# Kernel tuning notes

Hardware: AMD Instinct MI355X
Metric: run time of the kernel (lower is better)

Reference implementation:

```python
import jax, jax.numpy as jnp
import numpy as np

N_NODES = 50000
N_EDGES = 800000
N_GRAPHS = 128
HEADS = 4
HDIM = 32
N_CLASSES = 10
LEAKY_ALPHA = 0.2


def setup_inputs() -> dict:
    key = jax.random.key(0)
    ks = jax.random.split(key, 12)
    src = jax.random.randint(ks[0], (N_EDGES,), 0, N_NODES, dtype=jnp.int32)
    # guarantee every node has in-degree >= 1 so 3/deg is finite
    dst_tail = jax.random.randint(ks[1], (N_EDGES - N_NODES,), 0, N_NODES, dtype=jnp.int32)
    dst = jnp.concatenate([jnp.arange(N_NODES, dtype=jnp.int32), dst_tail])
    graph_ids = jnp.sort(jax.random.randint(ks[2], (N_NODES,), 0, N_GRAPHS, dtype=jnp.int32))
    s = 0.1
    return {
        "src": src,
        "dst": dst,
        "graph_ids": graph_ids,
        "W1": jax.random.normal(ks[3], (4, HEADS * HDIM), jnp.float32) * s,
        "al1": jax.random.normal(ks[4], (HEADS, HDIM), jnp.float32) * s,
        "ar1": jax.random.normal(ks[5], (HEADS, HDIM), jnp.float32) * s,
        "W2": jax.random.normal(ks[6], (HEADS * HDIM, HEADS * HDIM), jnp.float32) * s,
        "al2": jax.random.normal(ks[7], (HEADS, HDIM), jnp.float32) * s,
        "ar2": jax.random.normal(ks[8], (HEADS, HDIM), jnp.float32) * s,
        "Wc": jax.random.normal(ks[9], (HEADS * HDIM, N_CLASSES), jnp.float32) * s,
        "bc": jax.random.normal(ks[10], (N_CLASSES,), jnp.float32) * s,
    }


def _gat_layer(x, src, dst, W, al, ar):
    # x: [N, Fin]; W: [Fin, H*D]; al, ar: [H, D]
    n = x.shape[0]
    ft = (x @ W).reshape(n, HEADS, HDIM)                       # [N, H, D]
    a1 = jnp.einsum("nhd,hd->nh", ft, al)                      # [N, H]
    a2 = jnp.einsum("nhd,hd->nh", ft, ar)                      # [N, H]
    e = jax.nn.leaky_relu(a1[src] + a2[dst], LEAKY_ALPHA)      # [E, H]
    # segment softmax over incoming edges of each dst node
    m = jax.ops.segment_max(e, dst, num_segments=n)            # [N, H]
    m = jax.lax.stop_gradient(m)
    ex = jnp.exp(e - m[dst])                                   # [E, H]
    denom = jax.ops.segment_sum(ex, dst, num_segments=n)       # [N, H]
    alpha = ex / denom[dst]                                    # [E, H]
    # gather-multiply-scatter aggregation
    out = jax.ops.segment_sum(ft[src] * alpha[:, :, None], dst, num_segments=n)  # [N, H, D]
    return jax.nn.relu(out.reshape(n, HEADS * HDIM))


def reference(src, dst, graph_ids, W1, al1, ar1, W2, al2, ar2, Wc, bc):
    n = N_NODES
    ones_e = jnp.ones(src.shape[0], jnp.float32)
    deg = jax.ops.segment_sum(ones_e, dst, num_segments=n)     # in-degrees [N]
    h = jnp.stack(
        [deg, (deg - 3.0 > 0).astype(jnp.float32), 3.0 / deg, (deg - 4.0 > 0).astype(jnp.float32)],
        axis=1,
    )                                                          # [N, 4]
    h = _gat_layer(h, src, dst, W1, al1, ar1)                  # [N, H*D]
    h = _gat_layer(h, src, dst, W2, al2, ar2)                  # [N, H*D]
    # mean_nodes: per-graph mean pooling
    gsum = jax.ops.segment_sum(h, graph_ids, num_segments=N_GRAPHS)
    cnt = jax.ops.segment_sum(jnp.ones(n, jnp.float32), graph_ids, num_segments=N_GRAPHS)
    gmean = gsum / jnp.maximum(cnt, 1.0)[:, None]              # [G, H*D]
    return jax.nn.sigmoid(gmean @ Wc + bc)                     # [G, n_classes]
```

## Files before the change

### kernel.cpp

```cpp
#include <hip/hip_runtime.h>
#include <hip/hip_fp16.h>
#include <math.h>

#define HEADS 4
#define HDIM 32
#define FDIM 128
#define NGRAPH 128
#define NCLASS 10

#define NBW 128
#define NBP 512
#define SLICE 4096

typedef _Float16 h4_t __attribute__((ext_vector_type(4)));
typedef float f4_t __attribute__((ext_vector_type(4)));
typedef float f2_t __attribute__((ext_vector_type(2)));

__device__ __forceinline__ float lrelu(float x) { return fmaxf(x, 0.2f * x); }

__global__ void k_zb(int* __restrict__ bcnt) {
    int i = threadIdx.x;
    bcnt[i] = 0; bcnt[i + 256] = 0;
}

__global__ void k_bhist(const int* __restrict__ dst, int E, int* __restrict__ bcnt) {
    __shared__ int lcnt[NBP];
    int tid = threadIdx.x;
    for (int i = tid; i < NBP; i += 256) lcnt[i] = 0;
    __syncthreads();
    int beg = blockIdx.x * SLICE, end = min(E, beg + SLICE);
    for (int i = beg + tid; i < end; i += 256)
        atomicAdd(&lcnt[dst[i] >> 7], 1);
    __syncthreads();
    for (int i = tid; i < NBP; i += 256)
        if (lcnt[i]) atomicAdd(&bcnt[i], lcnt[i]);
}

__global__ void k_bscan2(const int* __restrict__ bcnt, int* __restrict__ bbase,
                         int* __restrict__ bcur) {
    __shared__ int ws[4];
    int tid = threadIdx.x, lane = tid & 63, w = tid >> 6;
    int c0 = bcnt[2 * tid], c1 = bcnt[2 * tid + 1];
    int t = c0 + c1;
    int incl = t;
    #pragma unroll
    for (int off = 1; off < 64; off <<= 1) {
        int y = __shfl_up(incl, off);
        if (lane >= off) incl += y;
    }
    if (lane == 63) ws[w] = incl;
    __syncthreads();
    int wpre = 0;
    #pragma unroll
    for (int j = 0; j < 4; ++j) if (j < w) wpre += ws[j];
    int ex = wpre + (incl - t);
    bbase[2 * tid] = ex;          bcur[2 * tid] = ex;
    bbase[2 * tid + 1] = ex + c0; bcur[2 * tid + 1] = ex + c0;
}

__global__ __launch_bounds__(256) void k_part(const int* __restrict__ src,
        const int* __restrict__ dst, int E, int* __restrict__ bcur,
        int2* __restrict__ part) {
    __shared__ int lcnt[NBP];
    __shared__ int loff[NBP];
    __shared__ int lpos[NBP];
    __shared__ int2 staged[SLICE];
    __shared__ int tgt[SLICE];
    __shared__ int ws[4];
    int tid = threadIdx.x, lane = tid & 63, w = tid >> 6;
    int beg = blockIdx.x * SLICE, end = min(E, beg + SLICE);
    int m = end - beg;
    for (int i = tid; i < NBP; i += 256) lcnt[i] = 0;
    __syncthreads();
    for (int i = beg + tid; i < end; i += 256)
        atomicAdd(&lcnt[dst[i] >> 7], 1);
    __syncthreads();
    int c0 = lcnt[2 * tid], c1 = lcnt[2 * tid + 1];
    int t = c0 + c1;
    int incl = t;
    #pragma unroll
    for (int off = 1; off < 64; off <<= 1) {
        int y = __shfl_up(incl, off);
        if (lane >= off) incl += y;
    }
    if (lane == 63) ws[w] = incl;
    __syncthreads();
    int wpre = 0;
    #pragma unroll
    for (int j = 0; j < 4; ++j) if (j < w) wpre += ws[j];
    int ex = wpre + (incl - t);
    loff[2 * tid] = ex; loff[2 * tid + 1] = ex + c0;
    if (c0) lpos[2 * tid] = atomicAdd(&bcur[2 * tid], c0);
    if (c1) lpos[2 * tid + 1] = atomicAdd(&bcur[2 * tid + 1], c1);
    lcnt[2 * tid] = 0; lcnt[2 * tid + 1] = 0;
    __syncthreads();
    for (int i = beg + tid; i < end; i += 256) {
        int s = src[i], d = dst[i];
        int b = d >> 7;
        int idx = atomicAdd(&lcnt[b], 1);
        int slot = loff[b] + idx;
        staged[slot] = make_int2(s, d);
        tgt[slot] = lpos[b] + idx;
    }
    __syncthreads();
    for (int i = tid; i < m; i += 256)
        part[tgt[i]] = staged[i];
}

__global__ __launch_bounds__(256) void k_build(const int2* __restrict__ part,
        const int* __restrict__ bbase, const int* __restrict__ bcnt,
        int* __restrict__ deg, int* __restrict__ offs, int* __restrict__ csr,
        int n, int E) {
    __shared__ int ldeg[NBW];
    __shared__ int loffs[NBW];
    __shared__ int wtot[2];
    int b = blockIdx.x, tid = threadIdx.x;
    int lane = tid & 63, w = tid >> 6;
    if (tid < NBW) ldeg[tid] = 0;
    __syncthreads();
    int beg = bbase[b], end = beg + bcnt[b];
    for (int i = beg + tid; i < end; i += 256)
        atomicAdd(&ldeg[part[i].y & (NBW - 1)], 1);
    __syncthreads();
    int x = (tid < NBW) ? ldeg[tid] : 0;
    int incl = x;
    #pragma unroll
    for (int off = 1; off < 64; off <<= 1) {
        int y = __shfl_up(incl, off);
        if (lane >= off) incl += y;
    }
    if (tid < NBW && lane == 63) wtot[w] = incl;
    __syncthreads();
    if (tid < NBW) {
        int pre = incl - x;
        if (w == 1) pre += wtot[0];
        loffs[tid] = beg + pre;
        int v = b * NBW + tid;
        if (v < n) { deg[v] = x; offs[v] = beg + pre; }
    }
    if (b == 0 && tid == 0) offs[n] = E;
    __syncthreads();
    if (tid < NBW) ldeg[tid] = 0;
    __syncthreads();
    for (int i = beg + tid; i < end; i += 256) {
        int2 e = part[i];
        int lv = e.y & (NBW - 1);
        int p = atomicAdd(&ldeg[lv], 1);
        csr[loffs[lv] + p] = e.x;
    }
}

__global__ void k_atts1(const int* __restrict__ deg, const float* __restrict__ W1,
                        const float* __restrict__ al, const float* __restrict__ ar,
                        float* __restrict__ h4t, float* __restrict__ a1,
                        float* __restrict__ a2, int n) {
    __shared__ float wla[16], wlr[16];
    int tid = threadIdx.x;
    if (tid < 32) {
        int k = (tid & 15) >> 2, h = tid & 3;
        const float* av = (tid < 16) ? al : ar;
        float s = 0.f;
        #pragma unroll
        for (int d = 0; d < 32; ++d) s += W1[k * FDIM + h * HDIM + d] * av[h * HDIM + d];
        if (tid < 16) wla[k * 4 + h] = s; else wlr[k * 4 + h] = s;
    }
    __syncthreads();
    int v = blockIdx.x * blockDim.x + tid;
    if (v >= n) return;
    float d = (float)deg[v];
    float4 hv = make_float4(d, (d - 3.0f > 0.0f) ? 1.0f : 0.0f, 3.0f / d,
                            (d - 4.0f > 0.0f) ? 1.0f : 0.0f);
    *(float4*)(h4t + v * 4) = hv;
    float4 o1, o2;
    #pragma unroll
    for (int h = 0; h < 4; ++h) {
        float s1 = hv.x * wla[0 + h] + hv.y * wla[4 + h] + hv.z * wla[8 + h] + hv.w * wla[12 + h];
        float s2 = hv.x * wlr[0 + h] + hv.y * wlr[4 + h] + hv.z * wlr[8 + h] + hv.w * wlr[12 + h];
        if (h == 0) { o1.x = s1; o2.x = s2; } else if (h == 1) { o1.y = s1; o2.y = s2; }
        else if (h == 2) { o1.z = s1; o2.z = s2; } else { o1.w = s1; o2.w = s2; }
    }
    *(float4*)(a1 + v * 4) = o1;
    *(float4*)(a2 + v * 4) = o2;
}

__global__ void k_agg1(const int* __restrict__ offs, const int* __restrict__ csr,
                       const float* __restrict__ h4t, const float* __restrict__ a1,
                       const float* __restrict__ a2, float* __restrict__ S, int n) {
    int tid = threadIdx.x, lane = tid & 63, w = tid >> 6;
    int g = lane >> 4, e = lane & 15;
    int v = (blockIdx.x * 4 + w) * 4 + g;
    bool vok = v < n;
    int beg = 0, end = 0;
    if (vok) { beg = offs[v]; end = offs[v + 1]; }
    int deg = end - beg;
    float4 a2v = vok ? *(const float4*)(a2 + v * 4) : make_float4(0, 0, 0, 0);
    float P[4][4]; float D[4];
    #pragma unroll
    for (int h = 0; h < 4; ++h) { D[h] = 0.f;
        #pragma unroll
        for (int d = 0; d < 4; ++d) P[h][d] = 0.f; }
    for (int base = 0; base < deg; base += 16) {
        if (base + e < deg) {
            int u = csr[beg + base + e];
            float4 a1u = *(const float4*)(a1 + u * 4);
            float4 f4  = *(const float4*)(h4t + u * 4);
            float wgt[4];
            wgt[0] = __expf(lrelu(a1u.x + a2v.x));
            wgt[1] = __expf(lrelu(a1u.y + a2v.y));
            wgt[2] = __expf(lrelu(a1u.z + a2v.z));
            wgt[3] = __expf(lrelu(a1u.w + a2v.w));
            #pragma unroll
            for (int h = 0; h < 4; ++h) {
                D[h] += wgt[h];
                P[h][0] = fmaf(wgt[h], f4.x, P[h][0]);
                P[h][1] = fmaf(wgt[h], f4.y, P[h][1]);
                P[h][2] = fmaf(wgt[h], f4.z, P[h][2]);
                P[h][3] = fmaf(wgt[h], f4.w, P[h][3]);
            }
        }
    }
    #pragma unroll
    for (int off = 1; off < 16; off <<= 1) {
        #pragma unroll
        for (int h = 0; h < 4; ++h) {
            D[h] += __shfl_xor(D[h], off);
            #pragma unroll
            for (int d = 0; d < 4; ++d) P[h][d] += __shfl_xor(P[h][d], off);
        }
    }
    if (vok && e == 0) {
        #pragma unroll
        for (int h = 0; h < 4; ++h) {
            float r = 1.0f / D[h];
            *(float4*)(S + v * 16 + h * 4) =
                make_float4(P[h][0] * r, P[h][1] * r, P[h][2] * r, P[h][3] * r);
        }
    }
}

__global__ void k_wfrag(const float* __restrict__ W2, __half* __restrict__ Wfrag,
                        float* __restrict__ gsum, int* __restrict__ gcnt) {
    int gid = blockIdx.x * 256 + threadIdx.x;
    ((float4*)gsum)[gid] = make_float4(0.f, 0.f, 0.f, 0.f);
    if (gid < NGRAPH) gcnt[gid] = 0;
    int fid = gid >> 6, l = gid & 63;
    int ks = fid >> 3, t = fid & 7;
    int k0 = ks * 16 + 4 * (l >> 4);
    int n0 = t * 16 + (l & 15);
    __half2 lo = __floats2half2_rn(W2[(k0 + 0) * FDIM + n0], W2[(k0 + 1) * FDIM + n0]);
    __half2 hi = __floats2half2_rn(W2[(k0 + 2) * FDIM + n0], W2[(k0 + 3) * FDIM + n0]);
    size_t base = ((size_t)fid * 64 + l) * 4;
    *(__half2*)(Wfrag + base)     = lo;
    *(__half2*)(Wfrag + base + 2) = hi;
}

__global__ __launch_bounds__(256) void k_layer2(const float* __restrict__ S,
        const float* __restrict__ W1, const __half* __restrict__ Wfrag,
        const float* __restrict__ al, const float* __restrict__ ar,
        unsigned char* __restrict__ ft8, float* __restrict__ a1,
        float* __restrict__ a2, int n) {
    __shared__ __half Blds[64 * 64 * 4];
    __shared__ __half Alds[4][16 * 132];
    int tid = threadIdx.x, l = tid & 63, w = tid >> 6;
    int c = l & 15, g = l >> 4;

    #pragma unroll
    for (int i = 0; i < 8; ++i)
        ((float4*)Blds)[i * 256 + tid] = ((const float4*)Wfrag)[i * 256 + tid];

    int v0 = (blockIdx.x * 4 + w) * 16;
    float2 w1c[4];
    #pragma unroll
    for (int d = 0; d < 4; ++d) w1c[d] = *(const float2*)(W1 + d * FDIM + 2 * l);
    for (int jj = 0; jj < 16; ++jj) {
        int v = min(v0 + jj, n - 1);
        float4 s = *(const float4*)(S + v * 16 + g * 4);
        float t0 = s.x * w1c[0].x + s.y * w1c[1].x + s.z * w1c[2].x + s.w * w1c[3].x;
        float t1 = s.x * w1c[0].y + s.y * w1c[1].y + s.z * w1c[2].y + s.w * w1c[3].y;
        *(__half2*)(&Alds[w][jj * 132 + 2 * l]) = __floats2half2_rn(fmaxf(t0, 0.f), fmaxf(t1, 0.f));
    }
    __syncthreads();

    f4_t acc[8];
    #pragma unroll
    for (int t = 0; t < 8; ++t) acc[t] = (f4_t){0.f, 0.f, 0.f, 0.f};
    #pragma unroll
    for (int ks = 0; ks < 8; ++ks) {
        h4_t af = *(const h4_t*)(&Alds[w][c * 132 + ks * 16 + 4 * g]);
        #pragma unroll
        for (int t = 0; t < 8; ++t) {
            h4_t bf = *(const h4_t*)(&Blds[((ks * 8 + t) * 64 + l) * 4]);
            acc[t] = __builtin_amdgcn_mfma_f32_16x16x16f16(af, bf, acc[t], 0, 0, 0);
        }
    }

    #pragma unroll
    for (int t = 0; t < 8; ++t) {
        #pragma unroll
        for (int r = 0; r < 4; ++r) {
            int v = v0 + 4 * g + r;
            if (v < n) {
                int pk = __builtin_amdgcn_cvt_pk_fp8_f32(acc[t][r], acc[t][r], 0, false);
                ft8[(size_t)v * FDIM + t * 16 + c] = (unsigned char)(pk & 0xff);
            }
        }
    }
    float al0[4], al1v[4], ar0[4], ar1v[4];
    #pragma unroll
    for (int h = 0; h < 4; ++h) {
        al0[h] = al[h * 32 + c]; al1v[h] = al[h * 32 + 16 + c];
        ar0[h] = ar[h * 32 + c]; ar1v[h] = ar[h * 32 + 16 + c];
    }
    #pragma unroll
    for (int r = 0; r < 4; ++r) {
        int v = v0 + 4 * g + r;
        #pragma unroll
        for (int h = 0; h < 4; ++h) {
            float p1 = acc[2 * h][r] * al0[h] + acc[2 * h + 1][r] * al1v[h];
            float p2 = acc[2 * h][r] * ar0[h] + acc[2 * h + 1][r] * ar1v[h];
            #pragma unroll
            for (int off = 1; off < 16; off <<= 1) {
                p1 += __shfl_xor(p1, off);
                p2 += __shfl_xor(p2, off);
            }
            if (c == h && v < n) {
                a1[v * 4 + h] = p1;
                a2[v * 4 + h] = p2;
            }
        }
    }
}

__global__ void k_agg2(const int* __restrict__ offs, const int* __restrict__ csr,
                       const unsigned char* __restrict__ ft8, const float* __restrict__ a1,
                       const float* __restrict__ a2, __half* __restrict__ out, int n) {
    __shared__ float wlds[4][64 * 4];
    int tid = threadIdx.x, lane = tid & 63, w = tid >> 6;
    int v = blockIdx.x * 4 + w;
    if (v >= n) return;
    int beg = offs[v], end = offs[v + 1];
    int deg = end - beg;
    float4 a2v = *(const float4*)(a2 + v * 4);
    int h = lane >> 4;
    int f = 2 * lane;
    float2 acc = make_float2(0.f, 0.f);
    float4 dsum = make_float4(0.f, 0.f, 0.f, 0.f);
    float* wbuf = wlds[w];
    for (int base = 0; base < deg; base += 64) {
        int m = min(64, deg - base);
        int u = 0;
        float4 wgt = make_float4(0.f, 0.f, 0.f, 0.f);
        if (lane < m) {
            u = csr[beg + base + lane];
            float4 a1u = *(const float4*)(a1 + u * 4);
            wgt.x = __expf(lrelu(a1u.x + a2v.x));
            wgt.y = __expf(lrelu(a1u.y + a2v.y));
            wgt.z = __expf(lrelu(a1u.z + a2v.z));
            wgt.w = __expf(lrelu(a1u.w + a2v.w));
        }
        dsum.x += wgt.x; dsum.y += wgt.y; dsum.z += wgt.z; dsum.w += wgt.w;
        *(float4*)(wbuf + lane * 4) = wgt;
        int j = 0;
        for (; j + 4 <= m; j += 4) {
            int s0 = __builtin_amdgcn_readlane(u, j);
            int s1 = __builtin_amdgcn_readlane(u, j + 1);
            int s2 = __builtin_amdgcn_readlane(u, j + 2);
            int s3 = __builtin_amdgcn_readlane(u, j + 3);
            float w0 = wbuf[(j + 0) * 4 + h];
            float w1 = wbuf[(j + 1) * 4 + h];
            float w2 = wbuf[(j + 2) * 4 + h];
            float w3 = wbuf[(j + 3) * 4 + h];
            int b0 = *(const unsigned short*)(ft8 + (size_t)s0 * FDIM + f);
            int b1 = *(const unsigned short*)(ft8 + (size_t)s1 * FDIM + f);
            int b2 = *(const unsigned short*)(ft8 + (size_t)s2 * FDIM + f);
            int b3 = *(const unsigned short*)(ft8 + (size_t)s3 * FDIM + f);
            f2_t g0 = __builtin_amdgcn_cvt_pk_f32_fp8(b0, false);
            f2_t g1 = __builtin_amdgcn_cvt_pk_f32_fp8(b1, false);
            f2_t g2 = __builtin_amdgcn_cvt_pk_f32_fp8(b2, false);
            f2_t g3 = __builtin_amdgcn_cvt_pk_f32_fp8(b3, false);
            acc.x = fmaf(w0, g0[0], acc.x); acc.y = fmaf(w0, g0[1], acc.y);
            acc.x = fmaf(w1, g1[0], acc.x); acc.y = fmaf(w1, g1[1], acc.y);
            acc.x = fmaf(w2, g2[0], acc.x); acc.y = fmaf(w2, g2[1], acc.y);
            acc.x = fmaf(w3, g3[0], acc.x); acc.y = fmaf(w3, g3[1], acc.y);
        }
        for (; j < m; ++j) {
            int s0 = __builtin_amdgcn_readlane(u, j);
            float w0 = wbuf[j * 4 + h];
            int b0 = *(const unsigned short*)(ft8 + (size_t)s0 * FDIM + f);
            f2_t g0 = __builtin_amdgcn_cvt_pk_f32_fp8(b0, false);
            acc.x = fmaf(w0, g0[0], acc.x); acc.y = fmaf(w0, g0[1], acc.y);
        }
    }
    #pragma unroll
    for (int off = 1; off < 64; off <<= 1) {
        dsum.x += __shfl_xor(dsum.x, off);
        dsum.y += __shfl_xor(dsum.y, off);
        dsum.z += __shfl_xor(dsum.z, off);
        dsum.w += __shfl_xor(dsum.w, off);
    }
    float dh = (h < 2) ? (h == 0 ? dsum.x : dsum.y) : (h == 2 ? dsum.z : dsum.w);
    float r = 1.0f / dh;
    *(__half2*)(out + (size_t)v * FDIM + f) =
        __floats2half2_rn(fmaxf(acc.x * r, 0.f), fmaxf(acc.y * r, 0.f));
}

__global__ void k_pool(const __half* __restrict__ hbuf, const int* __restrict__ gid,
                       float* __restrict__ gsum, int* __restrict__ gcnt, int n) {
    const int STRIP = 32;
    int wv = (blockIdx.x * blockDim.x + threadIdx.x) >> 6;
    int lane = threadIdx.x & 63;
    int beg = wv * STRIP;
    if (beg >= n) return;
    int end = min(beg + STRIP, n);
    int f = 2 * lane;
    float2 acc = make_float2(0.f, 0.f);
    int cur = gid[beg];
    int cnt = 0;
    for (int i = beg; i < end; ++i) {
        int g = gid[i];
        if (g != cur) {
            atomicAdd(&gsum[cur * FDIM + f], acc.x);
            atomicAdd(&gsum[cur * FDIM + f + 1], acc.y);
            if (lane == 0) atomicAdd(&gcnt[cur], cnt);
            acc = make_float2(0.f, 0.f); cnt = 0; cur = g;
        }
        float2 x = __half22float2(*(const __half2*)(hbuf + (size_t)i * FDIM + f));
        acc.x += x.x; acc.y += x.y; cnt++;
    }
    atomicAdd(&gsum[cur * FDIM + f], acc.x);
    atomicAdd(&gsum[cur * FDIM + f + 1], acc.y);
    if (lane == 0) atomicAdd(&gcnt[cur], cnt);
}

__global__ void k_classify(const float* __restrict__ gsum, const int* __restrict__ gcnt,
                           const float* __restrict__ Wc, const float* __restrict__ bc,
                           float* __restrict__ out) {
    int idx = blockIdx.x * blockDim.x + threadIdx.x;
    if (idx >= NGRAPH * NCLASS) return;
    int g = idx / NCLASS, c = idx % NCLASS;
    float rc = 1.0f / fmaxf((float)gcnt[g], 1.0f);
    float s = bc[c];
    for (int k = 0; k < FDIM; ++k)
        s += gsum[g * FDIM + k] * rc * Wc[k * NCLASS + c];
    out[idx] = 1.0f / (1.0f + __expf(-s));
}

extern "C" void kernel_launch(void* const* d_in, const int* in_sizes, int n_in,
                              void* d_out, int out_size, void* d_ws, size_t ws_size,
                              hipStream_t stream) {
    const int*   src = (const int*)d_in[0];
    const int*   dst = (const int*)d_in[1];
    const int*   gid = (const int*)d_in[2];
    const float* W1  = (const float*)d_in[3];
    const float* al1 = (const float*)d_in[4];
    const float* ar1 = (const float*)d_in[5];
    const float* W2  = (const float*)d_in[6];
    const float* al2 = (const float*)d_in[7];
    const float* ar2 = (const float*)d_in[8];
    const float* Wc  = (const float*)d_in[9];
    const float* bc  = (const float*)d_in[10];
    float* out = (float*)d_out;
    const int E = in_sizes[0];
    const int N = in_sizes[2];

    char* ws = (char*)d_ws;
    size_t off = 0;
    auto alloc = [&](size_t bytes) -> void* {
        void* p = ws + off;
        off = (off + bytes + 255) & ~(size_t)255;
        return p;
    };
    int*    deg    = (int*)alloc((size_t)N * 4);
    int*    offs   = (int*)alloc((size_t)(N + 1) * 4);
    int*    csr    = (int*)alloc((size_t)E * 4);
    int2*   part   = (int2*)alloc((size_t)E * 8);
    int*    bcnt   = (int*)alloc(NBP * 4);
    int*    bbase  = (int*)alloc(NBP * 4);
    int*    bcur   = (int*)alloc(NBP * 4);
    float*  h4t    = (float*)alloc((size_t)N * 4 * 4);
    float*  a1     = (float*)alloc((size_t)N * HEADS * 4);
    float*  a2     = (float*)alloc((size_t)N * HEADS * 4);
    float*  Sbuf   = (float*)alloc((size_t)N * 16 * 4);
    unsigned char* ft8 = (unsigned char*)alloc((size_t)N * FDIM);
    __half* hbuf   = (__half*)alloc((size_t)N * FDIM * 2);
    __half* Wfrag  = (__half*)alloc((size_t)FDIM * FDIM * 2);
    float*  gsum   = (float*)alloc((size_t)NGRAPH * FDIM * 4);
    int*    gcnt   = (int*)alloc((size_t)NGRAPH * 4);

    int pb_edges = (E + SLICE - 1) / SLICE;
    int nb2 = (N + NBW - 1) / NBW;

    k_zb<<<1, 256, 0, stream>>>(bcnt);
    k_bhist<<<pb_edges, 256, 0, stream>>>(dst, E, bcnt);
    k_bscan2<<<1, 256, 0, stream>>>(bcnt, bbase, bcur);
    k_part<<<pb_edges, 256, 0, stream>>>(src, dst, E, bcur, part);
    k_build<<<nb2, 256, 0, stream>>>(part, bbase, bcnt, deg, offs, csr, N, E);

    k_atts1<<<(N + 255) / 256, 256, 0, stream>>>(deg, W1, al1, ar1, h4t, a1, a2, N);
    k_agg1<<<(N + 15) / 16, 256, 0, stream>>>(offs, csr, h4t, a1, a2, Sbuf, N);
    k_wfrag<<<16, 256, 0, stream>>>(W2, Wfrag, gsum, gcnt);
    k_layer2<<<(N + 63) / 64, 256, 0, stream>>>(Sbuf, W1, Wfrag, al2, ar2, ft8, a1, a2, N);
    k_agg2<<<(N + 3) / 4, 256, 0, stream>>>(offs, csr, ft8, a1, a2, hbuf, N);

    int pb = (((N + 31) / 32) + 3) / 4;
    k_pool<<<pb, 256, 0, stream>>>(hbuf, gid, gsum, gcnt, N);
    k_classify<<<(NGRAPH * NCLASS + 255) / 256, 256, 0, stream>>>(gsum, gcnt, Wc, bc, out);
}
```

Baseline: 142.0 us.

## Fuse layer-1 attention into CSR build and layer-1 aggregation into layer-2 GEMM

```diff
diff --git a/kernel.cpp b/kernel.cpp
--- a/kernel.cpp
+++ b/kernel.cpp
@@ -18,9 +18,22 @@
 
 __device__ __forceinline__ float lrelu(float x) { return fmaxf(x, 0.2f * x); }
 
-__global__ void k_zb(int* __restrict__ bcnt) {
-    int i = threadIdx.x;
-    bcnt[i] = 0; bcnt[i + 256] = 0;
+__global__ void k_wfrag(const float* __restrict__ W2, __half* __restrict__ Wfrag,
+                        float* __restrict__ gsum, int* __restrict__ gcnt,
+                        int* __restrict__ bcnt) {
+    int gid = blockIdx.x * 256 + threadIdx.x;
+    ((float4*)gsum)[gid] = make_float4(0.f, 0.f, 0.f, 0.f);
+    if (gid < NGRAPH) gcnt[gid] = 0;
+    if (gid < NBP) bcnt[gid] = 0;
+    int fid = gid >> 6, l = gid & 63;
+    int ks = fid >> 3, t = fid & 7;
+    int k0 = ks * 16 + 4 * (l >> 4);
+    int n0 = t * 16 + (l & 15);
+    __half2 lo = __floats2half2_rn(W2[(k0 + 0) * FDIM + n0], W2[(k0 + 1) * FDIM + n0]);
+    __half2 hi = __floats2half2_rn(W2[(k0 + 2) * FDIM + n0], W2[(k0 + 3) * FDIM + n0]);
+    size_t base = ((size_t)fid * 64 + l) * 4;
+    *(__half2*)(Wfrag + base)     = lo;
+    *(__half2*)(Wfrag + base + 2) = hi;
 }
 
 __global__ void k_bhist(const int* __restrict__ dst, int E, int* __restrict__ bcnt) {
@@ -109,14 +122,25 @@
 
 __global__ __launch_bounds__(256) void k_build(const int2* __restrict__ part,
         const int* __restrict__ bbase, const int* __restrict__ bcnt,
-        int* __restrict__ deg, int* __restrict__ offs, int* __restrict__ csr,
+        const float* __restrict__ W1, const float* __restrict__ al,
+        const float* __restrict__ ar, int* __restrict__ offs, int* __restrict__ csr,
+        float* __restrict__ h4t, float* __restrict__ a1, float* __restrict__ a2,
         int n, int E) {
     __shared__ int ldeg[NBW];
     __shared__ int loffs[NBW];
     __shared__ int wtot[2];
+    __shared__ float wla[16], wlr[16];
     int b = blockIdx.x, tid = threadIdx.x;
     int lane = tid & 63, w = tid >> 6;
     if (tid < NBW) ldeg[tid] = 0;
+    if (tid < 32) {
+        int k = (tid & 15) >> 2, h = tid & 3;
+        const float* av = (tid < 16) ? al : ar;
+        float s = 0.f;
+        #pragma unroll
+        for (int d = 0; d < 32; ++d) s += W1[k * FDIM + h * HDIM + d] * av[h * HDIM + d];
+        if (tid < 16) wla[k * 4 + h] = s; else wlr[k * 4 + h] = s;
+    }
     __syncthreads();
     int beg = bbase[b], end = beg + bcnt[b];
     for (int i = beg + tid; i < end; i += 256)
@@ -136,7 +160,23 @@
         if (w == 1) pre += wtot[0];
         loffs[tid] = beg + pre;
         int v = b * NBW + tid;
-        if (v < n) { deg[v] = x; offs[v] = beg + pre; }
+        if (v < n) {
+            offs[v] = beg + pre;
+            float d = (float)x;
+            float4 hv = make_float4(d, (d - 3.0f > 0.0f) ? 1.0f : 0.0f, 3.0f / d,
+                                    (d - 4.0f > 0.0f) ? 1.0f : 0.0f);
+            *(float4*)(h4t + v * 4) = hv;
+            float4 o1, o2;
+            #pragma unroll
+            for (int h = 0; h < 4; ++h) {
+                float s1 = hv.x * wla[0 + h] + hv.y * wla[4 + h] + hv.z * wla[8 + h] + hv.w * wla[12 + h];
+                float s2 = hv.x * wlr[0 + h] + hv.y * wlr[4 + h] + hv.z * wlr[8 + h] + hv.w * wlr[12 + h];
+                if (h == 0) { o1.x = s1; o2.x = s2; } else if (h == 1) { o1.y = s1; o2.y = s2; }
+                else if (h == 2) { o1.z = s1; o2.z = s2; } else { o1.w = s1; o2.w = s2; }
+            }
+            *(float4*)(a1 + v * 4) = o1;
+            *(float4*)(a2 + v * 4) = o2;
+        }
     }
     if (b == 0 && tid == 0) offs[n] = E;
     __syncthreads();
@@ -150,131 +190,82 @@
     }
 }
 
-__global__ void k_atts1(const int* __restrict__ deg, const float* __restrict__ W1,
-                        const float* __restrict__ al, const float* __restrict__ ar,
-                        float* __restrict__ h4t, float* __restrict__ a1,
-                        float* __restrict__ a2, int n) {
-    __shared__ float wla[16], wlr[16];
-    int tid = threadIdx.x;
-    if (tid < 32) {
-        int k = (tid & 15) >> 2, h = tid & 3;
-        const float* av = (tid < 16) ? al : ar;
-        float s = 0.f;
-        #pragma unroll
-        for (int d = 0; d < 32; ++d) s += W1[k * FDIM + h * HDIM + d] * av[h * HDIM + d];
-        if (tid < 16) wla[k * 4 + h] = s; else wlr[k * 4 + h] = s;
-    }
-    __syncthreads();
-    int v = blockIdx.x * blockDim.x + tid;
-    if (v >= n) return;
-    float d = (float)deg[v];
-    float4 hv = make_float4(d, (d - 3.0f > 0.0f) ? 1.0f : 0.0f, 3.0f / d,
-                            (d - 4.0f > 0.0f) ? 1.0f : 0.0f);
-    *(float4*)(h4t + v * 4) = hv;
-    float4 o1, o2;
-    #pragma unroll
-    for (int h = 0; h < 4; ++h) {
-        float s1 = hv.x * wla[0 + h] + hv.y * wla[4 + h] + hv.z * wla[8 + h] + hv.w * wla[12 + h];
-        float s2 = hv.x * wlr[0 + h] + hv.y * wlr[4 + h] + hv.z * wlr[8 + h] + hv.w * wlr[12 + h];
-        if (h == 0) { o1.x = s1; o2.x = s2; } else if (h == 1) { o1.y = s1; o2.y = s2; }
-        else if (h == 2) { o1.z = s1; o2.z = s2; } else { o1.w = s1; o2.w = s2; }
-    }
-    *(float4*)(a1 + v * 4) = o1;
-    *(float4*)(a2 + v * 4) = o2;
-}
-
-__global__ void k_agg1(const int* __restrict__ offs, const int* __restrict__ csr,
-                       const float* __restrict__ h4t, const float* __restrict__ a1,
-                       const float* __restrict__ a2, float* __restrict__ S, int n) {
-    int tid = threadIdx.x, lane = tid & 63, w = tid >> 6;
-    int g = lane >> 4, e = lane & 15;
-    int v = (blockIdx.x * 4 + w) * 4 + g;
-    bool vok = v < n;
-    int beg = 0, end = 0;
-    if (vok) { beg = offs[v]; end = offs[v + 1]; }
-    int deg = end - beg;
-    float4 a2v = vok ? *(const float4*)(a2 + v * 4) : make_float4(0, 0, 0, 0);
-    float P[4][4]; float D[4];
-    #pragma unroll
-    for (int h = 0; h < 4; ++h) { D[h] = 0.f;
-        #pragma unroll
-        for (int d = 0; d < 4; ++d) P[h][d] = 0.f; }
-    for (int base = 0; base < deg; base += 16) {
-        if (base + e < deg) {
-            int u = csr[beg + base + e];
-            float4 a1u = *(const float4*)(a1 + u * 4);
-            float4 f4  = *(const float4*)(h4t + u * 4);
-            float wgt[4];
-            wgt[0] = __expf(lrelu(a1u.x + a2v.x));
-            wgt[1] = __expf(lrelu(a1u.y + a2v.y));
-            wgt[2] = __expf(lrelu(a1u.z + a2v.z));
-            wgt[3] = __expf(lrelu(a1u.w + a2v.w));
+__global__ __launch_bounds__(256) void k_l2f(const int* __restrict__ offs,
+        const int* __restrict__ csr, const float* __restrict__ h4t,
+        const float* __restrict__ a1, const float* __restrict__ a2,
+        const float* __restrict__ W1, const __half* __restrict__ Wfrag,
+        const float* __restrict__ al, const float* __restrict__ ar,
+        unsigned char* __restrict__ ft8, float* __restrict__ a1b,
+        float* __restrict__ a2b, int n) {
+    __shared__ __half Blds[64 * 64 * 4];
+    __shared__ __half Alds[4][16 * 132];
+    __shared__ float Slds[4][256];
+    int tid = threadIdx.x, l = tid & 63, w = tid >> 6;
+    int c = l & 15, g = l >> 4;
+
+    #pragma unroll
+    for (int i = 0; i < 8; ++i)
+        ((float4*)Blds)[i * 256 + tid] = ((const float4*)Wfrag)[i * 256 + tid];
+
+    int v0 = (blockIdx.x * 4 + w) * 16;
+
+    for (int r4 = 0; r4 < 4; ++r4) {
+        int v = v0 + r4 * 4 + g;
+        bool vok = v < n;
+        int beg = 0, end = 0;
+        if (vok) { beg = offs[v]; end = offs[v + 1]; }
+        int dg = end - beg;
+        float4 a2v = vok ? *(const float4*)(a2 + v * 4) : make_float4(0, 0, 0, 0);
+        float P[4][4], D[4];
+        #pragma unroll
+        for (int h = 0; h < 4; ++h) { D[h] = 0.f;
+            #pragma unroll
+            for (int d = 0; d < 4; ++d) P[h][d] = 0.f; }
+        for (int base2 = 0; base2 < dg; base2 += 16) {
+            if (base2 + c < dg) {
+                int u = csr[beg + base2 + c];
+                float4 a1u = *(const float4*)(a1 + u * 4);
+                float4 f4  = *(const float4*)(h4t + u * 4);
+                float wgt[4];
+                wgt[0] = __expf(lrelu(a1u.x + a2v.x));
+                wgt[1] = __expf(lrelu(a1u.y + a2v.y));
+                wgt[2] = __expf(lrelu(a1u.z + a2v.z));
+                wgt[3] = __expf(lrelu(a1u.w + a2v.w));
+                #pragma unroll
+                for (int h = 0; h < 4; ++h) {
+                    D[h] += wgt[h];
+                    P[h][0] = fmaf(wgt[h], f4.x, P[h][0]);
+                    P[h][1] = fmaf(wgt[h], f4.y, P[h][1]);
+                    P[h][2] = fmaf(wgt[h], f4.z, P[h][2]);
+                    P[h][3] = fmaf(wgt[h], f4.w, P[h][3]);
+                }
+            }
+        }
+        #pragma unroll
+        for (int off = 1; off < 16; off <<= 1) {
             #pragma unroll
             for (int h = 0; h < 4; ++h) {
-                D[h] += wgt[h];
-                P[h][0] = fmaf(wgt[h], f4.x, P[h][0]);
-                P[h][1] = fmaf(wgt[h], f4.y, P[h][1]);
-                P[h][2] = fmaf(wgt[h], f4.z, P[h][2]);
-                P[h][3] = fmaf(wgt[h], f4.w, P[h][3]);
-            }
-        }
-    }
-    #pragma unroll
-    for (int off = 1; off < 16; off <<= 1) {
-        #pragma unroll
-        for (int h = 0; h < 4; ++h) {
-            D[h] += __shfl_xor(D[h], off);
+                D[h] += __shfl_xor(D[h], off);
+                #pragma unroll
+                for (int d = 0; d < 4; ++d) P[h][d] += __shfl_xor(P[h][d], off);
+            }
+        }
+        if (vok && c == 0) {
             #pragma unroll
-            for (int d = 0; d < 4; ++d) P[h][d] += __shfl_xor(P[h][d], off);
-        }
-    }
-    if (vok && e == 0) {
-        #pragma unroll
-        for (int h = 0; h < 4; ++h) {
-            float r = 1.0f / D[h];
-            *(float4*)(S + v * 16 + h * 4) =
-                make_float4(P[h][0] * r, P[h][1] * r, P[h][2] * r, P[h][3] * r);
-        }
-    }
-}
-
-__global__ void k_wfrag(const float* __restrict__ W2, __half* __restrict__ Wfrag,
-                        float* __restrict__ gsum, int* __restrict__ gcnt) {
-    int gid = blockIdx.x * 256 + threadIdx.x;
-    ((float4*)gsum)[gid] = make_float4(0.f, 0.f, 0.f, 0.f);
-    if (gid < NGRAPH) gcnt[gid] = 0;
-    int fid = gid >> 6, l = gid & 63;
-    int ks = fid >> 3, t = fid & 7;
-    int k0 = ks * 16 + 4 * (l >> 4);
-    int n0 = t * 16 + (l & 15);
-    __half2 lo = __floats2half2_rn(W2[(k0 + 0) * FDIM + n0], W2[(k0 + 1) * FDIM + n0]);
-    __half2 hi = __floats2half2_rn(W2[(k0 + 2) * FDIM + n0], W2[(k0 + 3) * FDIM + n0]);
-    size_t base = ((size_t)fid * 64 + l) * 4;
-    *(__half2*)(Wfrag + base)     = lo;
-    *(__half2*)(Wfrag + base + 2) = hi;
-}
-
-__global__ __launch_bounds__(256) void k_layer2(const float* __restrict__ S,
-        const float* __restrict__ W1, const __half* __restrict__ Wfrag,
-        const float* __restrict__ al, const float* __restrict__ ar,
-        unsigned char* __restrict__ ft8, float* __restrict__ a1,
-        float* __restrict__ a2, int n) {
-    __shared__ __half Blds[64 * 64 * 4];
-    __shared__ __half Alds[4][16 * 132];
-    int tid = threadIdx.x, l = tid & 63, w = tid >> 6;
-    int c = l & 15, g = l >> 4;
-
-    #pragma unroll
-    for (int i = 0; i < 8; ++i)
-        ((float4*)Blds)[i * 256 + tid] = ((const float4*)Wfrag)[i * 256 + tid];
-
-    int v0 = (blockIdx.x * 4 + w) * 16;
+            for (int h = 0; h < 4; ++h) {
+                float r = 1.0f / D[h];
+                #pragma unroll
+                for (int d = 0; d < 4; ++d)
+                    Slds[w][(r4 * 4 + g) * 16 + h * 4 + d] = P[h][d] * r;
+            }
+        }
+    }
+
     float2 w1c[4];
     #pragma unroll
     for (int d = 0; d < 4; ++d) w1c[d] = *(const float2*)(W1 + d * FDIM + 2 * l);
     for (int jj = 0; jj < 16; ++jj) {
-        int v = min(v0 + jj, n - 1);
-        float4 s = *(const float4*)(S + v * 16 + g * 4);
+        float4 s = *(const float4*)(&Slds[w][jj * 16 + g * 4]);
         float t0 = s.x * w1c[0].x + s.y * w1c[1].x + s.z * w1c[2].x + s.w * w1c[3].x;
         float t1 = s.x * w1c[0].y + s.y * w1c[1].y + s.z * w1c[2].y + s.w * w1c[3].y;
         *(__half2*)(&Alds[w][jj * 132 + 2 * l]) = __floats2half2_rn(fmaxf(t0, 0.f), fmaxf(t1, 0.f));
@@ -324,8 +315,8 @@
                 p2 += __shfl_xor(p2, off);
             }
             if (c == h && v < n) {
-                a1[v * 4 + h] = p1;
-                a2[v * 4 + h] = p2;
+                a1b[v * 4 + h] = p1;
+                a2b[v * 4 + h] = p2;
             }
         }
     }
@@ -470,7 +461,6 @@
         off = (off + bytes + 255) & ~(size_t)255;
         return p;
     };
-    int*    deg    = (int*)alloc((size_t)N * 4);
     int*    offs   = (int*)alloc((size_t)(N + 1) * 4);
     int*    csr    = (int*)alloc((size_t)E * 4);
     int2*   part   = (int2*)alloc((size_t)E * 8);
@@ -480,7 +470,8 @@
     float*  h4t    = (float*)alloc((size_t)N * 4 * 4);
     float*  a1     = (float*)alloc((size_t)N * HEADS * 4);
     float*  a2     = (float*)alloc((size_t)N * HEADS * 4);
-    float*  Sbuf   = (float*)alloc((size_t)N * 16 * 4);
+    float*  a1b    = (float*)alloc((size_t)N * HEADS * 4);
+    float*  a2b    = (float*)alloc((size_t)N * HEADS * 4);
     unsigned char* ft8 = (unsigned char*)alloc((size_t)N * FDIM);
     __half* hbuf   = (__half*)alloc((size_t)N * FDIM * 2);
     __half* Wfrag  = (__half*)alloc((size_t)FDIM * FDIM * 2);
@@ -490,17 +481,15 @@
     int pb_edges = (E + SLICE - 1) / SLICE;
     int nb2 = (N + NBW - 1) / NBW;
 
-    k_zb<<<1, 256, 0, stream>>>(bcnt);
+    k_wfrag<<<16, 256, 0, stream>>>(W2, Wfrag, gsum, gcnt, bcnt);
     k_bhist<<<pb_edges, 256, 0, stream>>>(dst, E, bcnt);
     k_bscan2<<<1, 256, 0, stream>>>(bcnt, bbase, bcur);
     k_part<<<pb_edges, 256, 0, stream>>>(src, dst, E, bcur, part);
-    k_build<<<nb2, 256, 0, stream>>>(part, bbase, bcnt, deg, offs, csr, N, E);
-
-    k_atts1<<<(N + 255) / 256, 256, 0, stream>>>(deg, W1, al1, ar1, h4t, a1, a2, N);
-    k_agg1<<<(N + 15) / 16, 256, 0, stream>>>(offs, csr, h4t, a1, a2, Sbuf, N);
-    k_wfrag<<<16, 256, 0, stream>>>(W2, Wfrag, gsum, gcnt);
-    k_layer2<<<(N + 63) / 64, 256, 0, stream>>>(Sbuf, W1, Wfrag, al2, ar2, ft8, a1, a2, N);
-    k_agg2<<<(N + 3) / 4, 256, 0, stream>>>(offs, csr, ft8, a1, a2, hbuf, N);
+    k_build<<<nb2, 256, 0, stream>>>(part, bbase, bcnt, W1, al1, ar1,
+                                     offs, csr, h4t, a1, a2, N, E);
+    k_l2f<<<(N + 63) / 64, 256, 0, stream>>>(offs, csr, h4t, a1, a2, W1, Wfrag,
+                                             al2, ar2, ft8, a1b, a2b, N);
+    k_agg2<<<(N + 3) / 4, 256, 0, stream>>>(offs, csr, ft8, a1b, a2b, hbuf, N);
 
     int pb = (((N + 31) / 32) + 3) / 4;
     k_pool<<<pb, 256, 0, stream>>>(hbuf, gid, gsum, gcnt, N);
```

After: 140.7 us. No clear change (-0.9%).
